# Performance work log

Measured on AMD Instinct MI355X. Metric: run time of the kernel, lower is better.

## Reference

```python
import jax, jax.numpy as jnp
from jax import lax
import numpy as np

N = 10000      # nodes
T = 60         # lookback window
F = 16         # features per timestep
HL = 256       # lstm hidden dim
GH = 8         # gat heads
GC = 64        # gat out channels per head
GD = GH * GC   # 512 concat dim
FH = 512       # fusion hidden
E = 320000     # edges (before self loops)


def _lstm_layer(x, w_ih, w_hh, b_ih, b_hh):
    # x: [T, N, in] -> hidden sequence [T, N, HL]; torch gate order i,f,g,o
    n = x.shape[1]
    h0 = jnp.zeros((n, HL), x.dtype)
    def step(carry, xt):
        h, c = carry
        g = xt @ w_ih.T + h @ w_hh.T + b_ih + b_hh
        i, f, gg, o = jnp.split(g, 4, axis=-1)
        c = jax.nn.sigmoid(f) * c + jax.nn.sigmoid(i) * jnp.tanh(gg)
        h = jax.nn.sigmoid(o) * jnp.tanh(c)
        return (h, c), h
    _, hs = lax.scan(step, (h0, h0), x)
    return hs


def _gatv2(x, src, dst, ea, wl, bl, wr, br, we, att, bias):
    # GATv2Conv (concat=True, edge_dim=1, negative_slope=0.2); self loops already in src/dst/ea
    n = x.shape[0]
    xl = (x @ wl + bl).reshape(n, GH, GC)   # lin_l (source / x_j)
    xr = (x @ wr + br).reshape(n, GH, GC)   # lin_r (target / x_i)
    ee = (ea @ we).reshape(-1, GH, GC)      # lin_edge (bias=False)
    m = jax.nn.leaky_relu(xl[src] + xr[dst] + ee, 0.2)      # [E', GH, GC]
    logits = jnp.einsum('ehc,hc->eh', m, att)               # [E', GH]
    mx = jax.ops.segment_max(logits, dst, num_segments=n)
    ex = jnp.exp(logits - mx[dst])
    den = jax.ops.segment_sum(ex, dst, num_segments=n)
    alpha = ex / den[dst]                                   # softmax over in-edges per node
    out = jax.ops.segment_sum(xl[src] * alpha[..., None], dst, num_segments=n)
    return out.reshape(n, GD) + bias


def setup_inputs():
    key = jax.random.key(0)
    ks = jax.random.split(key, 20)
    f32 = jnp.float32
    def nrm(k, shp, fan):
        return jax.random.normal(k, shp, f32) * (1.0 / np.sqrt(fan))
    return {
        "x_seq": jax.random.normal(ks[0], (N, T, F), f32),
        "edge_index": jax.random.randint(ks[1], (2, E), 0, N, jnp.int32),
        "edge_attr": jax.random.uniform(ks[2], (E, 1), dtype=f32),
        "w_ih0": nrm(ks[3], (4 * HL, F), HL), "w_hh0": nrm(ks[4], (4 * HL, HL), HL),
        "b_ih0": jnp.zeros((4 * HL,), f32), "b_hh0": jnp.zeros((4 * HL,), f32),
        "w_ih1": nrm(ks[5], (4 * HL, HL), HL), "w_hh1": nrm(ks[6], (4 * HL, HL), HL),
        "b_ih1": jnp.zeros((4 * HL,), f32), "b_hh1": jnp.zeros((4 * HL,), f32),
        "g0_wl": nrm(ks[7], (HL, GD), HL), "g0_bl": jnp.zeros((GD,), f32),
        "g0_wr": nrm(ks[8], (HL, GD), HL), "g0_br": jnp.zeros((GD,), f32),
        "g0_we": nrm(ks[9], (1, GD), 1),
        "g0_att": nrm(ks[10], (GH, GC), GC), "g0_bias": jnp.zeros((GD,), f32),
        "g1_wl": nrm(ks[11], (GD, GD), GD), "g1_bl": jnp.zeros((GD,), f32),
        "g1_wr": nrm(ks[12], (GD, GD), GD), "g1_br": jnp.zeros((GD,), f32),
        "g1_we": nrm(ks[13], (1, GD), 1),
        "g1_att": nrm(ks[14], (GH, GC), GC), "g1_bias": jnp.zeros((GD,), f32),
        "fc1_w": nrm(ks[15], (HL + GD, FH), HL + GD), "fc1_b": jnp.zeros((FH,), f32),
        "fc2_w": nrm(ks[16], (FH, 1), FH), "fc2_b": jnp.zeros((1,), f32),
    }


def reference(x_seq, edge_index, edge_attr,
              w_ih0, w_hh0, b_ih0, b_hh0, w_ih1, w_hh1, b_ih1, b_hh1,
              g0_wl, g0_bl, g0_wr, g0_br, g0_we, g0_att, g0_bias,
              g1_wl, g1_bl, g1_wr, g1_br, g1_we, g1_att, g1_bias,
              fc1_w, fc1_b, fc2_w, fc2_b):
    # 2-layer LSTM encoder, take last timestep hidden (dropout off: eval mode)
    xt = jnp.transpose(x_seq, (1, 0, 2))            # [T, N, F]
    h1 = _lstm_layer(xt, w_ih0, w_hh0, b_ih0, b_hh0)
    h2 = _lstm_layer(h1, w_ih1, w_hh1, b_ih1, b_hh1)
    node = h2[-1]                                    # [N, HL]
    # add self loops; fill edge_attr for loops with mean (PyG default fill_value='mean')
    loop = jnp.arange(N, dtype=edge_index.dtype)
    src = jnp.concatenate([edge_index[0], loop])
    dst = jnp.concatenate([edge_index[1], loop])
    ea = jnp.concatenate([edge_attr, jnp.broadcast_to(edge_attr.mean(axis=0), (N, 1))], axis=0)
    g = jax.nn.elu(_gatv2(node, src, dst, ea, g0_wl, g0_bl, g0_wr, g0_br, g0_we, g0_att, g0_bias))
    g = jax.nn.elu(_gatv2(g, src, dst, ea, g1_wl, g1_bl, g1_wr, g1_br, g1_we, g1_att, g1_bias))
    fused = jnp.concatenate([node, g], axis=1)       # [N, HL+GD]
    h = jax.nn.relu(fused @ fc1_w + fc1_b)
    return h @ fc2_w + fc2_b                         # [N, 1]
```

## Files before the change

### kernel.cpp

```cpp
#include <hip/hip_runtime.h>

#define DEV __device__ __forceinline__

typedef _Float16 f16;
typedef _Float16 f16x8 __attribute__((ext_vector_type(8)));
typedef _Float16 f16x2 __attribute__((ext_vector_type(2)));
typedef float f32x4 __attribute__((ext_vector_type(4)));

DEV float sigmoidf_(float x) { return 1.0f / (1.0f + __expf(-x)); }
DEV float tanhf2_(float x)   { return 1.0f - 2.0f / (__expf(2.0f * x) + 1.0f); }

DEV void load_lds16(const void* g, void* l) {
    __builtin_amdgcn_global_load_lds(
        (const __attribute__((address_space(1))) char*)(const char*)g,
        (__attribute__((address_space(3))) char*)(unsigned int)(unsigned long long)(char*)l,
        16, 0, 0);
}

DEV int swz(int row, int ck) { return ck ^ (row & 3) ^ ((row >> 2) & 3); }

__global__ void prep_w0_kernel(const float* __restrict__ wih,
                               const float* __restrict__ whh,
                               f16* __restrict__ dst) {
    int idx = blockIdx.x * 256 + threadIdx.x;
    if (idx >= 1024 * 288) return;
    int rd = idx / 288, k = idx - rd * 288;
    int T = rd >> 7, p = rd & 127;
    int u = T * 32 + ((p >> 6) & 1) * 16 + (p & 15);
    int g = (p >> 4) & 3;
    int src = g * 256 + u;
    float v;
    if (k < 16)        v = wih[src * 16 + k];
    else if (k < 272)  v = whh[src * 256 + (k - 16)];
    else               v = 0.f;
    dst[idx] = (f16)v;
}

__global__ void prep_w1_kernel(const float* __restrict__ wih,
                               const float* __restrict__ whh,
                               f16* __restrict__ dst) {
    int idx = blockIdx.x * 256 + threadIdx.x;
    if (idx >= 1024 * 512) return;
    int rd = idx >> 9, k = idx & 511;
    int T = rd >> 7, p = rd & 127;
    int u = T * 32 + ((p >> 6) & 1) * 16 + (p & 15);
    int g = (p >> 4) & 3;
    int src = g * 256 + u;
    float v = (k < 256) ? wih[src * 256 + k] : whh[src * 256 + (k - 256)];
    dst[idx] = (f16)v;
}

__global__ void prep_bias4_kernel(const float* __restrict__ bi,
                                  const float* __restrict__ bh,
                                  float* __restrict__ dst) {
    int idx = blockIdx.x * 256 + threadIdx.x;
    if (idx >= 1024) return;
    int u = idx >> 2, g = idx & 3;
    dst[idx] = bi[g * 256 + u] + bh[g * 256 + u];
}

__global__ void prep_wt_kernel(const float* __restrict__ src, f16* __restrict__ dst,
                               int K, int N) {
    int idx = blockIdx.x * 256 + threadIdx.x;
    if (idx >= K * N) return;
    int n = idx / K, k = idx - n * K;
    dst[idx] = (f16)src[(size_t)k * N + n];
}

__global__ void prep_x0_kernel(const float* __restrict__ x_seq, f16* __restrict__ A0,
                               int Nn) {
    int idx = blockIdx.x * 256 + threadIdx.x;
    if (idx >= Nn * 16) return;
    int m = idx >> 4, f = idx & 15;
    A0[(size_t)m * 288 + f] = (f16)x_seq[(size_t)m * 960 + f];
}

DEV void tile_load_chunk(const f16* __restrict__ A, int lda,
                         const f16* __restrict__ Bt, int K,
                         int m0, int n0, int k0,
                         f16* __restrict__ sA, f16* __restrict__ sB,
                         int w, int arow, int achk)
{
#pragma unroll
    for (int c = 0; c < 2; ++c) {
        int R = c * 64 + w * 16;
        load_lds16(A + (size_t)(m0 + R + arow) * lda + k0 + achk, sA + R * 32);
        load_lds16(Bt + (size_t)(n0 + R + arow) * K + k0 + achk, sB + R * 32);
    }
}

DEV void tile_compute_chunk(const f16* __restrict__ sA, const f16* __restrict__ sB,
                            f32x4 (&acc)[4][4], int wr, int wc, int frow, int fsl)
{
    f16x8 af[4], bf[4];
#pragma unroll
    for (int i = 0; i < 4; ++i)
        af[i] = *(const f16x8*)&sA[(wr + i * 16 + frow) * 32 + fsl];
#pragma unroll
    for (int j = 0; j < 4; ++j)
        bf[j] = *(const f16x8*)&sB[(wc + j * 16 + frow) * 32 + fsl];
#pragma unroll
    for (int i = 0; i < 4; ++i)
#pragma unroll
        for (int j = 0; j < 4; ++j)
            acc[i][j] = __builtin_amdgcn_mfma_f32_16x16x32_f16(af[i], bf[j], acc[i][j], 0, 0, 0);
}

DEV void lstm_step_core(
    f16* __restrict__ sA, f16* __restrict__ sB,
    int bx, int by,
    const f16* __restrict__ A, int lda, int K,
    const f16* __restrict__ Wt,
    const float* __restrict__ bias4,
    float* __restrict__ c_state,
    f16* __restrict__ hA, int ldhA, int offhA,
    f16* __restrict__ hB, int ldhB, int offhB,
    const float* __restrict__ xsrc, int tnext,
    int M)
{
    const int tid = threadIdx.x;
    const int w = tid >> 6, lane = tid & 63;
    const int m0 = bx * 128, n0 = by * 128;
    const int arow = lane >> 2;
    const int achk = swz(arow, lane & 3) * 8;
    const int frow = lane & 15, l4 = lane >> 4;
    const int fsl = swz(frow, l4) * 8;
    const int wr = (w >> 1) * 64, wc = (w & 1) * 64;

    const int u = by * 32 + (w & 1) * 16 + (lane & 15);
    const int rbase = m0 + wr + (lane >> 4) * 4;
    float cold[4][4];
#pragma unroll
    for (int i = 0; i < 4; ++i)
#pragma unroll
        for (int r = 0; r < 4; ++r)
            cold[i][r] = c_state[(size_t)(rbase + i * 16 + r) * 256 + u];

    f32x4 acc[4][4] = {};
    const int nch = K >> 5;

    tile_load_chunk(A, lda, Wt, K, m0, n0, 0, sA, sB, w, arow, achk);
    for (int kc = 0; kc < nch; ++kc) {
        __syncthreads();
        const int cur = (kc & 1) * 4096;
        if (kc + 1 < nch) {
            const int nxt = ((kc + 1) & 1) * 4096;
            tile_load_chunk(A, lda, Wt, K, m0, n0, (kc + 1) * 32,
                            sA + nxt, sB + nxt, w, arow, achk);
        }
        tile_compute_chunk(sA + cur, sB + cur, acc, wr, wc, frow, fsl);
    }

    const float4 bb = *(const float4*)&bias4[u * 4];
#pragma unroll
    for (int i = 0; i < 4; ++i) {
#pragma unroll
        for (int r = 0; r < 4; ++r) {
            int m = rbase + i * 16 + r;
            if (m < M) {
                float gi = sigmoidf_(acc[i][0][r] + bb.x);
                float gf = sigmoidf_(acc[i][1][r] + bb.y);
                float gg = tanhf2_(acc[i][2][r] + bb.z);
                float go = sigmoidf_(acc[i][3][r] + bb.w);
                float cn = gf * cold[i][r] + gi * gg;
                c_state[(size_t)m * 256 + u] = cn;
                f16 h = (f16)(go * tanhf2_(cn));
                hA[(size_t)m * ldhA + offhA + u] = h;
                if (hB) hB[(size_t)m * ldhB + offhB + u] = h;
            }
        }
    }
    if (xsrc && by == 0) {
        int row = tid >> 1, fb = (tid & 1) * 8;
        int m = m0 + row;
        if (m < M) {
            const float* xp = xsrc + (size_t)m * 960 + tnext * 16 + fb;
            f16* dp = hB + (size_t)m * ldhB + fb;
#pragma unroll
            for (int q = 0; q < 8; ++q) dp[q] = (f16)xp[q];
        }
    }
}

__global__ __launch_bounds__(256) void lstm_mfma_kernel(
    const f16* __restrict__ A, int lda, int K,
    const f16* __restrict__ Wt, const float* __restrict__ bias4,
    float* __restrict__ c_state,
    f16* __restrict__ hA, int ldhA, int offhA,
    f16* __restrict__ hB, int ldhB, int offhB,
    const float* __restrict__ xsrc, int tnext, int M, int mtiles)
{
    __shared__ __align__(16) f16 sA[2 * 4096];
    __shared__ __align__(16) f16 sB[2 * 4096];
    const int l = blockIdx.x;
    const int xcd = l & 7, q = l >> 3;
    const int y = q & 7, xhi = q >> 3;
    const int x = xhi * 8 + xcd;
    if (x >= mtiles) return;
    lstm_step_core(sA, sB, x, y, A, lda, K, Wt, bias4, c_state,
                   hA, ldhA, offhA, hB, ldhB, offhB, xsrc, tnext, M);
}

__global__ __launch_bounds__(256) void lstm_dual_kernel(
    const f16* __restrict__ A1, const f16* __restrict__ W1t,
    const float* __restrict__ b41, float* __restrict__ c1,
    f16* __restrict__ h1A, int ldh1A, int offh1A,
    const f16* __restrict__ A0, const f16* __restrict__ W0t,
    const float* __restrict__ b40, float* __restrict__ c0,
    f16* __restrict__ h0A, int ldh0A, int offh0A,
    f16* __restrict__ h0B, int ldh0B, int offh0B,
    const float* __restrict__ xsrc, int tnext, int M, int mtiles)
{
    __shared__ __align__(16) f16 sA[2 * 4096];
    __shared__ __align__(16) f16 sB[2 * 4096];
    const int l = blockIdx.x;
    const int xcd = l & 7, q = l >> 3;
    const int yz = q & 15, xhi = q >> 4;
    const int x = xhi * 8 + xcd;
    if (x >= mtiles) return;
    const int y = yz & 7, z = yz >> 3;
    if (z == 0)
        lstm_step_core(sA, sB, x, y, A1, 512, 512, W1t, b41, c1,
                       h1A, ldh1A, offh1A, nullptr, 0, 0, nullptr, 0, M);
    else
        lstm_step_core(sA, sB, x, y, A0, 288, 288, W0t, b40, c0,
                       h0A, ldh0A, offh0A, h0B, ldh0B, offh0B, xsrc, tnext, M);
}

__global__ __launch_bounds__(256) void gemm16_kernel(
    const f16* __restrict__ A, int lda,
    const f16* __restrict__ Bt, int K,
    const float* __restrict__ bias,
    f16* __restrict__ C16, float* __restrict__ C32, int ldc,
    int act, int M)
{
    __shared__ __align__(16) f16 sA[2 * 4096];
    __shared__ __align__(16) f16 sB[2 * 4096];
    const int tid = threadIdx.x;
    const int w = tid >> 6, lane = tid & 63;
    const int m0 = blockIdx.x * 128, n0 = blockIdx.y * 128;
    const int arow = lane >> 2;
    const int achk = swz(arow, lane & 3) * 8;
    const int frow = lane & 15, l4 = lane >> 4;
    const int fsl = swz(frow, l4) * 8;
    const int wr = (w >> 1) * 64, wcn = (w & 1) * 64;

    f32x4 acc[4][4] = {};
    const int nch = K >> 5;

    tile_load_chunk(A, lda, Bt, K, m0, n0, 0, sA, sB, w, arow, achk);
    for (int kc = 0; kc < nch; ++kc) {
        __syncthreads();
        const int cur = (kc & 1) * 4096;
        if (kc + 1 < nch) {
            const int nxt = ((kc + 1) & 1) * 4096;
            tile_load_chunk(A, lda, Bt, K, m0, n0, (kc + 1) * 32,
                            sA + nxt, sB + nxt, w, arow, achk);
        }
        tile_compute_chunk(sA + cur, sB + cur, acc, wr, wcn, frow, fsl);
    }

    const int rbase = m0 + wr + (lane >> 4) * 4;
#pragma unroll
    for (int i = 0; i < 4; ++i) {
#pragma unroll
        for (int r = 0; r < 4; ++r) {
            int m = rbase + i * 16 + r;
            if (m >= M) continue;
#pragma unroll
            for (int j = 0; j < 4; ++j) {
                int n = n0 + wcn + j * 16 + (lane & 15);
                float v = acc[i][j][r] + bias[n];
                if (act == 1) v = fmaxf(v, 0.f);
                if (C16) C16[(size_t)m * ldc + n] = (f16)v;
                else     C32[(size_t)m * ldc + n] = v;
            }
        }
    }
}

__global__ __launch_bounds__(256) void gemm16_dual_kernel(
    const f16* __restrict__ A, int lda,
    const f16* __restrict__ Btl, const f16* __restrict__ Btr, int K,
    const float* __restrict__ biasl, const float* __restrict__ biasr,
    f16* __restrict__ Cl, f16* __restrict__ Cr, int ldc, int M)
{
    __shared__ __align__(16) f16 sA[2 * 4096];
    __shared__ __align__(16) f16 sB[2 * 4096];
    const int side = blockIdx.y >> 2;
    const f16* Bt = side ? Btr : Btl;
    const float* bias = side ? biasr : biasl;
    f16* C16 = side ? Cr : Cl;
    const int tid = threadIdx.x;
    const int w = tid >> 6, lane = tid & 63;
    const int m0 = blockIdx.x * 128, n0 = (blockIdx.y & 3) * 128;
    const int arow = lane >> 2;
    const int achk = swz(arow, lane & 3) * 8;
    const int frow = lane & 15, l4 = lane >> 4;
    const int fsl = swz(frow, l4) * 8;
    const int wr = (w >> 1) * 64, wcn = (w & 1) * 64;

    f32x4 acc[4][4] = {};
    const int nch = K >> 5;

    tile_load_chunk(A, lda, Bt, K, m0, n0, 0, sA, sB, w, arow, achk);
    for (int kc = 0; kc < nch; ++kc) {
        __syncthreads();
        const int cur = (kc & 1) * 4096;
        if (kc + 1 < nch) {
            const int nxt = ((kc + 1) & 1) * 4096;
            tile_load_chunk(A, lda, Bt, K, m0, n0, (kc + 1) * 32,
                            sA + nxt, sB + nxt, w, arow, achk);
        }
        tile_compute_chunk(sA + cur, sB + cur, acc, wr, wcn, frow, fsl);
    }

    const int rbase = m0 + wr + (lane >> 4) * 4;
#pragma unroll
    for (int i = 0; i < 4; ++i) {
#pragma unroll
        for (int r = 0; r < 4; ++r) {
            int m = rbase + i * 16 + r;
            if (m >= M) continue;
#pragma unroll
            for (int j = 0; j < 4; ++j) {
                int n = n0 + wcn + j * 16 + (lane & 15);
                float v = acc[i][j][r] + bias[n];
                C16[(size_t)m * ldc + n] = (f16)v;
            }
        }
    }
}

__global__ void mean_sum_kernel(const float* __restrict__ a, int n, float* __restrict__ out) {
    __shared__ float s[256];
    float loc = 0.f;
    for (int i = blockIdx.x * 256 + threadIdx.x; i < n; i += gridDim.x * 256) loc += a[i];
    s[threadIdx.x] = loc;
    __syncthreads();
    for (int off = 128; off; off >>= 1) {
        if (threadIdx.x < off) s[threadIdx.x] += s[threadIdx.x + off];
        __syncthreads();
    }
    if (threadIdx.x == 0) atomicAdd(out, s[0]);
}

__global__ void hist_kernel(const int* __restrict__ ei, int Ne, int Nn,
                            int* __restrict__ counts) {
    int e = blockIdx.x * 256 + threadIdx.x;
    if (e >= Ne + Nn) return;
    int d = (e < Ne) ? ei[Ne + e] : (e - Ne);
    atomicAdd(&counts[d], 1);
}

__global__ void scan_kernel(const int* __restrict__ counts, int* __restrict__ offsets, int n) {
    __shared__ int s[256];
    int tid = threadIdx.x;
    int chunk = (n + 255) / 256;
    int b = tid * chunk;
    int loc = 0;
    for (int j = 0; j < chunk; ++j) { int i = b + j; if (i < n) loc += counts[i]; }
    s[tid] = loc;
    __syncthreads();
    for (int off = 1; off < 256; off <<= 1) {
        int v = (tid >= off) ? s[tid - off] : 0;
        __syncthreads();
        s[tid] += v;
        __syncthreads();
    }
    int run = (tid == 0) ? 0 : s[tid - 1];
    for (int j = 0; j < chunk; ++j) {
        int i = b + j;
        if (i < n) { offsets[i] = run; run += counts[i]; }
    }
    if (tid == 255) offsets[n] = run;
}

__global__ void scatter_kernel(const int* __restrict__ ei, const float* __restrict__ ea,
                               const float* __restrict__ sump, float inv_ne, int Ne, int Nn,
                               int* __restrict__ cursor, int* __restrict__ src_sorted,
                               float* __restrict__ ea_sorted) {
    int e = blockIdx.x * 256 + threadIdx.x;
    if (e >= Ne + Nn) return;
    int s, d; float a;
    if (e < Ne) { s = ei[e]; d = ei[Ne + e]; a = ea[e]; }
    else        { s = e - Ne; d = s; a = sump[0] * inv_ne; }
    int pos = atomicAdd(&cursor[d], 1);
    src_sorted[pos] = s;
    ea_sorted[pos] = a;
}

__global__ __launch_bounds__(256) void gat_fused_kernel(
    const f16* __restrict__ xl, const f16* __restrict__ xr,
    const float* __restrict__ we, const float* __restrict__ att,
    const float* __restrict__ bias,
    const int* __restrict__ offsets, const int* __restrict__ src_sorted,
    const float* __restrict__ ea_sorted,
    f16* __restrict__ out, int ldo, int N)
{
    const int i = blockIdx.x;
    const int tid = threadIdx.x;
    const int c2 = tid * 2;

    f16x2 xrv = *(const f16x2*)&xr[(size_t)i * 512 + c2];
    const float xr0 = (float)xrv.x, xr1 = (float)xrv.y;
    const float we0 = we[c2], we1 = we[c2 + 1];
    const float at0 = att[c2], at1 = att[c2 + 1];

    const int beg = offsets[i], end = offsets[i + 1];

    float m = -1e30f, den = 0.f, acc0 = 0.f, acc1 = 0.f;

    float a = ea_sorted[beg];
    f16x2 xv = *(const f16x2*)&xl[(size_t)src_sorted[beg] * 512 + c2];

    for (int e = beg; e < end; ++e) {
        float an = a; f16x2 xvn = xv;
        if (e + 1 < end) {
            int sn = src_sorted[e + 1];
            an = ea_sorted[e + 1];
            xvn = *(const f16x2*)&xl[(size_t)sn * 512 + c2];
        }
        float x0 = (float)xv.x, x1 = (float)xv.y;
        float v0 = x0 + xr0 + a * we0;
        float v1 = x1 + xr1 + a * we1;
        v0 = (v0 > 0.f) ? v0 : 0.2f * v0;
        v1 = (v1 > 0.f) ? v1 : 0.2f * v1;
        float p = v0 * at0 + v1 * at1;
        p += __shfl_xor(p, 1);
        p += __shfl_xor(p, 2);
        p += __shfl_xor(p, 4);
        p += __shfl_xor(p, 8);
        p += __shfl_xor(p, 16);
        float mn = fmaxf(m, p);
        float r  = __expf(m - mn);
        float wg = __expf(p - mn);
        acc0 = acc0 * r + wg * x0;
        acc1 = acc1 * r + wg * x1;
        den  = den * r + wg;
        m = mn;
        a = an; xv = xvn;
    }

    float rden = 1.f / den;
    float v0 = acc0 * rden + bias[c2];
    float v1 = acc1 * rden + bias[c2 + 1];
    v0 = (v0 > 0.f) ? v0 : __expf(v0) - 1.f;
    v1 = (v1 > 0.f) ? v1 : __expf(v1) - 1.f;
    f16x2 ov; ov.x = (f16)v0; ov.y = (f16)v1;
    *(f16x2*)&out[(size_t)i * ldo + c2] = ov;
}

__global__ void fc2_kernel(const float* __restrict__ H, const float* __restrict__ w,
                           const float* __restrict__ b, float* __restrict__ out, int N) {
    int wv = threadIdx.x >> 6, lane = threadIdx.x & 63;
    int node = blockIdx.x * 4 + wv;
    if (node >= N) return;
    float s = 0.f;
#pragma unroll
    for (int j = 0; j < 8; ++j)
        s += H[(size_t)node * 512 + j * 64 + lane] * w[j * 64 + lane];
#pragma unroll
    for (int off = 32; off; off >>= 1) s += __shfl_xor(s, off, 64);
    if (lane == 0) out[node] = s + b[0];
}

extern "C" void kernel_launch(void* const* d_in, const int* in_sizes, int n_in,
                              void* d_out, int out_size, void* d_ws, size_t ws_size,
                              hipStream_t stream) {
    const float* x_seq     = (const float*)d_in[0];
    const int*   edge_index= (const int*)d_in[1];
    const float* edge_attr = (const float*)d_in[2];
    const float* w_ih0 = (const float*)d_in[3];
    const float* w_hh0 = (const float*)d_in[4];
    const float* b_ih0 = (const float*)d_in[5];
    const float* b_hh0 = (const float*)d_in[6];
    const float* w_ih1 = (const float*)d_in[7];
    const float* w_hh1 = (const float*)d_in[8];
    const float* b_ih1 = (const float*)d_in[9];
    const float* b_hh1 = (const float*)d_in[10];
    const float* g0_wl = (const float*)d_in[11];
    const float* g0_bl = (const float*)d_in[12];
    const float* g0_wr = (const float*)d_in[13];
    const float* g0_br = (const float*)d_in[14];
    const float* g0_we = (const float*)d_in[15];
    const float* g0_att= (const float*)d_in[16];
    const float* g0_bias=(const float*)d_in[17];
    const float* g1_wl = (const float*)d_in[18];
    const float* g1_bl = (const float*)d_in[19];
    const float* g1_wr = (const float*)d_in[20];
    const float* g1_br = (const float*)d_in[21];
    const float* g1_we = (const float*)d_in[22];
    const float* g1_att= (const float*)d_in[23];
    const float* g1_bias=(const float*)d_in[24];
    const float* fc1_w = (const float*)d_in[25];
    const float* fc1_b = (const float*)d_in[26];
    const float* fc2_w = (const float*)d_in[27];
    const float* fc2_b = (const float*)d_in[28];
    float* out = (float*)d_out;

    const int Nn = in_sizes[0] / (60 * 16);
    const int Ne = in_sizes[1] / 2;
    const int Etot = Ne + Nn;
    const int MT = (Nn + 127) / 128;
    const int Mpad = MT * 128;
    const int MTpad8 = ((MT + 7) / 8) * 8;

    size_t off = 0;
    auto alloc = [&](size_t bytes) -> void* {
        void* r = (char*)d_ws + off;
        off += (bytes + 255) & ~(size_t)255;
        return r;
    };
    f16* W0t   = (f16*)alloc((size_t)1024 * 288 * 2);
    f16* W1t   = (f16*)alloc((size_t)1024 * 512 * 2);
    float* b40 = (float*)alloc(1024 * 4);
    float* b41 = (float*)alloc(1024 * 4);
    f16* Wg0l  = (f16*)alloc((size_t)512 * 256 * 2);
    f16* Wg0r  = (f16*)alloc((size_t)512 * 256 * 2);
    f16* Wg1l  = (f16*)alloc((size_t)512 * 512 * 2);
    f16* Wg1r  = (f16*)alloc((size_t)512 * 512 * 2);
    f16* Wfc1  = (f16*)alloc((size_t)512 * 768 * 2);
    f16* A0b[2]; A0b[0] = (f16*)alloc((size_t)Mpad * 288 * 2);
                 A0b[1] = (f16*)alloc((size_t)Mpad * 288 * 2);
    f16* A1b[2]; A1b[0] = (f16*)alloc((size_t)Mpad * 512 * 2);
                 A1b[1] = (f16*)alloc((size_t)Mpad * 512 * 2);
    float* c0  = (float*)alloc((size_t)Mpad * 256 * 4);
    float* c1  = (float*)alloc((size_t)Mpad * 256 * 4);
    f16* fused = (f16*)alloc((size_t)Mpad * 768 * 2);
    f16* xlbuf = (f16*)alloc((size_t)Mpad * 512 * 2);
    f16* xrbuf = (f16*)alloc((size_t)Mpad * 512 * 2);
    f16* gbuf  = (f16*)alloc((size_t)Mpad * 512 * 2);
    float* hfc1= (float*)alloc((size_t)Mpad * 512 * 4);
    int* counts  = (int*)alloc((size_t)Nn * 4);
    int* offsets = (int*)alloc((size_t)(Nn + 1) * 4);
    int* cursor  = (int*)alloc((size_t)Nn * 4);
    int* src_sorted = (int*)alloc((size_t)Etot * 4);
    float* ea_sorted = (float*)alloc((size_t)Etot * 4);
    float* meanp = (float*)alloc(256);

    prep_w0_kernel<<<dim3((1024 * 288 + 255) / 256), 256, 0, stream>>>(w_ih0, w_hh0, W0t);
    prep_w1_kernel<<<dim3((1024 * 512 + 255) / 256), 256, 0, stream>>>(w_ih1, w_hh1, W1t);
    prep_bias4_kernel<<<dim3(4), 256, 0, stream>>>(b_ih0, b_hh0, b40);
    prep_bias4_kernel<<<dim3(4), 256, 0, stream>>>(b_ih1, b_hh1, b41);
    prep_wt_kernel<<<dim3((256 * 512 + 255) / 256), 256, 0, stream>>>(g0_wl, Wg0l, 256, 512);
    prep_wt_kernel<<<dim3((256 * 512 + 255) / 256), 256, 0, stream>>>(g0_wr, Wg0r, 256, 512);
    prep_wt_kernel<<<dim3((512 * 512 + 255) / 256), 256, 0, stream>>>(g1_wl, Wg1l, 512, 512);
    prep_wt_kernel<<<dim3((512 * 512 + 255) / 256), 256, 0, stream>>>(g1_wr, Wg1r, 512, 512);
    prep_wt_kernel<<<dim3((768 * 512 + 255) / 256), 256, 0, stream>>>(fc1_w, Wfc1, 768, 512);
    hipMemsetAsync(A0b[0], 0, (size_t)Mpad * 288 * 2, stream);
    hipMemsetAsync(A0b[1], 0, (size_t)Mpad * 288 * 2, stream);
    hipMemsetAsync(A1b[0], 0, (size_t)Mpad * 512 * 2, stream);
    hipMemsetAsync(c0, 0, (size_t)Mpad * 256 * 4, stream);
    hipMemsetAsync(c1, 0, (size_t)Mpad * 256 * 4, stream);
    prep_x0_kernel<<<dim3((Nn * 16 + 255) / 256), 256, 0, stream>>>(x_seq, A0b[0], Nn);

    hipMemsetAsync(meanp, 0, 4, stream);
    hipMemsetAsync(counts, 0, (size_t)Nn * 4, stream);
    mean_sum_kernel<<<dim3(256), 256, 0, stream>>>(edge_attr, Ne, meanp);
    hist_kernel<<<dim3((Etot + 255) / 256), 256, 0, stream>>>(edge_index, Ne, Nn, counts);
    scan_kernel<<<dim3(1), 256, 0, stream>>>(counts, offsets, Nn);
    hipMemcpyAsync(cursor, offsets, (size_t)Nn * 4, hipMemcpyDeviceToDevice, stream);
    scatter_kernel<<<dim3((Etot + 255) / 256), 256, 0, stream>>>(
        edge_index, edge_attr, meanp, 1.0f / (float)Ne, Ne, Nn, cursor, src_sorted, ea_sorted);

    const int solo_grid = MTpad8 * 8;
    const int dual_grid = MTpad8 * 16;
    lstm_mfma_kernel<<<dim3(solo_grid), 256, 0, stream>>>(
        A0b[0], 288, 288, W0t, b40, c0,
        A1b[0], 512, 0,
        A0b[1], 288, 16,
        x_seq, 1, Nn, MT);
    for (int k = 0; k < 59; ++k) {
        lstm_dual_kernel<<<dim3(dual_grid), 256, 0, stream>>>(
            A1b[k & 1], W1t, b41, c1,
            A1b[(k + 1) & 1], 512, 256,
            A0b[(k + 1) & 1], W0t, b40, c0,
            A1b[(k + 1) & 1], 512, 0,
            A0b[k & 1], 288, 16,
            (k + 1 < 59) ? x_seq : nullptr, k + 2, Nn, MT);
    }
    lstm_mfma_kernel<<<dim3(solo_grid), 256, 0, stream>>>(
        A1b[1], 512, 512, W1t, b41, c1,
        fused, 768, 0,
        nullptr, 0, 0,
        nullptr, 0, Nn, MT);

    gemm16_dual_kernel<<<dim3(MT, 8), 256, 0, stream>>>(
        fused, 768, Wg0l, Wg0r, 256, g0_bl, g0_br, xlbuf, xrbuf, 512, Nn);
    gat_fused_kernel<<<dim3(Nn), 256, 0, stream>>>(
        xlbuf, xrbuf, g0_we, g0_att, g0_bias, offsets, src_sorted, ea_sorted,
        gbuf, 512, Nn);

    gemm16_dual_kernel<<<dim3(MT, 8), 256, 0, stream>>>(
        gbuf, 512, Wg1l, Wg1r, 512, g1_bl, g1_br, xlbuf, xrbuf, 512, Nn);
    gat_fused_kernel<<<dim3(Nn), 256, 0, stream>>>(
        xlbuf, xrbuf, g1_we, g1_att, g1_bias, offsets, src_sorted, ea_sorted,
        fused + 256, 768, Nn);

    gemm16_kernel<<<dim3(MT, 4), 256, 0, stream>>>(
        fused, 768, Wfc1, 768, fc1_b, nullptr, hfc1, 512, 1, Nn);
    fc2_kernel<<<dim3((Nn + 3) / 4), 256, 0, stream>>>(hfc1, fc2_w, fc2_b, out, Nn);
}
```

Before: 2.943 ms.

## Split GAT edge loop across four waves with wide loads and lazy rescaling

The fused GATv2 aggregation kernel now gives each wave a quarter of a node's in-edges. Each lane handles 8 channels with 16-byte loads, so the per-head reduction needs only 3 shuffles. A lazy online-softmax skips the exponential rescale whenever every lane's logit stays within a threshold of the running max. The per-wave partial max, denominator and accumulators are merged through LDS after a barrier, which adds shared-memory traffic and a synchronisation in exchange for more memory-level parallelism on the gathers.

```diff
diff --git a/kernel.cpp b/kernel.cpp
--- a/kernel.cpp
+++ b/kernel.cpp
@@ -398,53 +398,91 @@
     const float* __restrict__ ea_sorted,
     f16* __restrict__ out, int ldo, int N)
 {
+    __shared__ float s_acc[8][4][64];
+    __shared__ float s_m[4][64];
+    __shared__ float s_den[4][64];
     const int i = blockIdx.x;
     const int tid = threadIdx.x;
-    const int c2 = tid * 2;
-
-    f16x2 xrv = *(const f16x2*)&xr[(size_t)i * 512 + c2];
-    const float xr0 = (float)xrv.x, xr1 = (float)xrv.y;
-    const float we0 = we[c2], we1 = we[c2 + 1];
-    const float at0 = att[c2], at1 = att[c2 + 1];
+    const int w = tid >> 6, lane = tid & 63;
+    const int c8 = lane * 8;
+
+    f16x8 xrv = *(const f16x8*)&xr[(size_t)i * 512 + c8];
+    float xr_[8], we_[8], at_[8];
+#pragma unroll
+    for (int k = 0; k < 8; ++k) xr_[k] = (float)xrv[k];
+    *(float4*)&we_[0] = *(const float4*)&we[c8];
+    *(float4*)&we_[4] = *(const float4*)&we[c8 + 4];
+    *(float4*)&at_[0] = *(const float4*)&att[c8];
+    *(float4*)&at_[4] = *(const float4*)&att[c8 + 4];
 
     const int beg = offsets[i], end = offsets[i + 1];
 
-    float m = -1e30f, den = 0.f, acc0 = 0.f, acc1 = 0.f;
-
-    float a = ea_sorted[beg];
-    f16x2 xv = *(const f16x2*)&xl[(size_t)src_sorted[beg] * 512 + c2];
-
-    for (int e = beg; e < end; ++e) {
-        float an = a; f16x2 xvn = xv;
-        if (e + 1 < end) {
-            int sn = src_sorted[e + 1];
-            an = ea_sorted[e + 1];
-            xvn = *(const f16x2*)&xl[(size_t)sn * 512 + c2];
-        }
-        float x0 = (float)xv.x, x1 = (float)xv.y;
-        float v0 = x0 + xr0 + a * we0;
-        float v1 = x1 + xr1 + a * we1;
-        v0 = (v0 > 0.f) ? v0 : 0.2f * v0;
-        v1 = (v1 > 0.f) ? v1 : 0.2f * v1;
-        float p = v0 * at0 + v1 * at1;
+    float m = -1e30f, den = 0.f;
+    float acc[8] = {};
+
+    int e = beg + w;
+    float a = 0.f; f16x8 xv = {};
+    if (e < end) {
+        a = ea_sorted[e];
+        xv = *(const f16x8*)&xl[(size_t)src_sorted[e] * 512 + c8];
+    }
+    for (; e < end; e += 4) {
+        float an = a; f16x8 xvn = xv;
+        if (e + 4 < end) {
+            int sn = src_sorted[e + 4];
+            an = ea_sorted[e + 4];
+            xvn = *(const f16x8*)&xl[(size_t)sn * 512 + c8];
+        }
+        float x[8];
+        float p = 0.f;
+#pragma unroll
+        for (int k = 0; k < 8; ++k) {
+            x[k] = (float)xv[k];
+            float v = x[k] + xr_[k] + a * we_[k];
+            v = (v > 0.f) ? v : 0.2f * v;
+            p = fmaf(v, at_[k], p);
+        }
         p += __shfl_xor(p, 1);
         p += __shfl_xor(p, 2);
         p += __shfl_xor(p, 4);
-        p += __shfl_xor(p, 8);
-        p += __shfl_xor(p, 16);
-        float mn = fmaxf(m, p);
-        float r  = __expf(m - mn);
-        float wg = __expf(p - mn);
-        acc0 = acc0 * r + wg * x0;
-        acc1 = acc1 * r + wg * x1;
-        den  = den * r + wg;
-        m = mn;
+        if (__all(p <= m + 8.f)) {
+            float wg = __expf(p - m);
+            den += wg;
+#pragma unroll
+            for (int k = 0; k < 8; ++k) acc[k] = fmaf(wg, x[k], acc[k]);
+        } else {
+            float mn = fmaxf(m, p);
+            float r  = __expf(m - mn);
+            float wg = __expf(p - mn);
+            den = den * r + wg;
+#pragma unroll
+            for (int k = 0; k < 8; ++k) acc[k] = fmaf(acc[k], r, wg * x[k]);
+            m = mn;
+        }
         a = an; xv = xvn;
     }
 
-    float rden = 1.f / den;
-    float v0 = acc0 * rden + bias[c2];
-    float v1 = acc1 * rden + bias[c2 + 1];
+    s_m[w][lane] = m;
+    s_den[w][lane] = den;
+#pragma unroll
+    for (int k = 0; k < 8; ++k) s_acc[k][w][lane] = acc[k];
+    __syncthreads();
+
+    const int c2 = tid * 2;
+    const int l = c2 >> 3;
+    const int k0 = c2 & 7;
+    float m0 = s_m[0][l], m1 = s_m[1][l], m2 = s_m[2][l], m3 = s_m[3][l];
+    float M = fmaxf(fmaxf(m0, m1), fmaxf(m2, m3));
+    float e0 = __expf(m0 - M), e1 = __expf(m1 - M);
+    float e2 = __expf(m2 - M), e3 = __expf(m3 - M);
+    float D = s_den[0][l] * e0 + s_den[1][l] * e1 + s_den[2][l] * e2 + s_den[3][l] * e3;
+    float A0 = s_acc[k0][0][l] * e0 + s_acc[k0][1][l] * e1
+             + s_acc[k0][2][l] * e2 + s_acc[k0][3][l] * e3;
+    float A1 = s_acc[k0 + 1][0][l] * e0 + s_acc[k0 + 1][1][l] * e1
+             + s_acc[k0 + 1][2][l] * e2 + s_acc[k0 + 1][3][l] * e3;
+    float rD = 1.f / D;
+    float v0 = A0 * rD + bias[c2];
+    float v1 = A1 * rD + bias[c2 + 1];
     v0 = (v0 > 0.f) ? v0 : __expf(v0) - 1.f;
     v1 = (v1 > 0.f) ? v1 : __expf(v1) - 1.f;
     f16x2 ov; ov.x = (f16)v0; ov.y = (f16)v1;
```

New measurement: 2.822 ms. 1.04x faster.
